# Optimization experiments

Hardware: AMD Instinct MI355X
Metric: run time of the kernel (lower is better)

Reference implementation:

```python
import jax, jax.numpy as jnp
import numpy as np

LN_EPS = 1e-5

def _layer_norm(x, g, b):
    mu = jnp.mean(x, axis=-1, keepdims=True)
    var = jnp.mean(jnp.square(x - mu), axis=-1, keepdims=True)
    return (x - mu) * jax.lax.rsqrt(var + LN_EPS) * g + b

def _conv(x, src, tgt, N, alphas, ws, W3, W_self, bias, deg_power):
    # alphas, ws: tuples of 3 per-edge [E] arrays (sp, ctx, lat)
    # W3: [3, in, out]; deg_power: [3]
    out = x @ W_self + bias  # self loop + bias, [N, out]
    for c in range(3):
        eff = alphas[c] * ws[c]                                   # [E]
        deg = jnp.ones((N,), x.dtype).at[tgt].add(eff)            # [N]
        dinv = jnp.power(jnp.clip(deg, 1e-6), deg_power[c])       # [N]
        norm = eff * dinv[tgt] * dinv[src]                        # [E]
        h = x @ W3[c]                                             # [N, out] (linear => transform before gather)
        msg = norm[:, None] * h[src]                              # [E, out]
        out = out + jax.ops.segment_sum(msg, tgt, num_segments=N)
    return out

def setup_inputs() -> dict:
    N, E, D, L = 50000, 1000000, 128, 2
    key = jax.random.key(0)
    ks = jax.random.split(key, 16)
    scale = 1.0 / np.sqrt(D)
    inp = {
        "x": jax.random.normal(ks[0], (N, D), jnp.float32),
        "edge_index": jax.random.randint(ks[1], (2, E), 0, N, jnp.int32),
        "alpha_sp": jax.random.uniform(ks[2], (E,), jnp.float32),
        "alpha_ctx": jax.random.uniform(ks[3], (E,), jnp.float32),
        "alpha_lat": jax.random.uniform(ks[4], (E,), jnp.float32),
        "w_sp": jax.random.uniform(ks[5], (E,), jnp.float32),
        "w_ctx": jax.random.uniform(ks[6], (E,), jnp.float32),
        "w_lat": jax.random.uniform(ks[7], (E,), jnp.float32),
        # stacked per-layer params: [L, 3, in, out] for the three channel weights
        "W3": jax.random.normal(ks[8], (L, 3, D, D), jnp.float32) * scale,
        "W_self": jax.random.normal(ks[9], (L, D, D), jnp.float32) * scale,
        "bias": jnp.zeros((L, D), jnp.float32),
        "deg_power": jnp.full((L, 3), -0.5, jnp.float32),
        "ln_g": jnp.ones((D,), jnp.float32),
        "ln_b": jnp.zeros((D,), jnp.float32),
        "num_nodes": N,
    }
    return inp

def reference(x, edge_index, alpha_sp, alpha_ctx, alpha_lat, w_sp, w_ctx, w_lat,
              W3, W_self, bias, deg_power, ln_g, ln_b, num_nodes):
    N = num_nodes
    src, tgt = edge_index[0], edge_index[1]
    alphas = (alpha_sp, alpha_ctx, alpha_lat)
    ws = (w_sp, w_ctx, w_lat)
    L = W3.shape[0]
    h = x
    for i in range(L):
        h = _conv(h, src, tgt, N, alphas, ws, W3[i], W_self[i], bias[i], deg_power[i])
        if i < L - 1:
            h = _layer_norm(h, ln_g, ln_b)
            h = jax.nn.relu(h)
            # dropout: eval mode (identity)
    return h
```

## Files before the change

kernel.cpp:

```cpp
#include <hip/hip_runtime.h>
#include <hip/hip_bf16.h>

typedef short bf16x8 __attribute__((ext_vector_type(8)));
typedef float f32x4 __attribute__((ext_vector_type(4)));

static inline int cdiv(int a, int b){ return (a + b - 1) / b; }

__device__ __forceinline__ unsigned pack_bf16_hi(float v){
    return ((unsigned)__bfloat16_as_ushort(__float2bfloat16(v))) << 16;
}
__device__ __forceinline__ float bf16hi_to_f32(unsigned bits_hi16){
    return __uint_as_float(bits_hi16);
}

__global__ void k_cnt(const int* __restrict__ tgt, int* __restrict__ cnt, int E){
    int e0 = (blockIdx.x * 256 + threadIdx.x) * 4;
    if (e0 + 3 < E){
        int4 t = *(const int4*)(tgt + e0);
        atomicAdd(&cnt[t.x], 1);
        atomicAdd(&cnt[t.y], 1);
        atomicAdd(&cnt[t.z], 1);
        atomicAdd(&cnt[t.w], 1);
    } else {
        for (int e = e0; e < E; ++e) atomicAdd(&cnt[tgt[e]], 1);
    }
}

__global__ void k_scan1(const int* __restrict__ cnt, int* __restrict__ rs,
                        int* __restrict__ bsum, int N){
    __shared__ int s[256];
    int i = blockIdx.x * 256 + threadIdx.x;
    int v = (i < N) ? cnt[i] : 0;
    s[threadIdx.x] = v;
    __syncthreads();
    for (int off = 1; off < 256; off <<= 1){
        int t = (threadIdx.x >= off) ? s[threadIdx.x - off] : 0;
        __syncthreads();
        s[threadIdx.x] += t;
        __syncthreads();
    }
    if (i < N) rs[i] = s[threadIdx.x] - v;
    if (threadIdx.x == 255) bsum[blockIdx.x] = s[255];
}

__global__ void k_scan2(int* __restrict__ bsum, int nb){
    __shared__ int s[256];
    int v = (threadIdx.x < nb) ? bsum[threadIdx.x] : 0;
    s[threadIdx.x] = v;
    __syncthreads();
    for (int off = 1; off < 256; off <<= 1){
        int t = (threadIdx.x >= off) ? s[threadIdx.x - off] : 0;
        __syncthreads();
        s[threadIdx.x] += t;
        __syncthreads();
    }
    if (threadIdx.x < nb) bsum[threadIdx.x] = s[threadIdx.x] - v;
}

__global__ void k_scan3(int* __restrict__ rs, int* __restrict__ nxt,
                        const int* __restrict__ bsum, int N, int E){
    int i = blockIdx.x * 256 + threadIdx.x;
    if (i < N){
        int v = rs[i] + bsum[blockIdx.x];
        rs[i] = v;
        nxt[i] = v;
    }
    if (i == 0) rs[N] = E;
}

__global__ void k_scatter(const int* __restrict__ src, const int* __restrict__ tgt,
                          const float* __restrict__ asp,
                          const float* __restrict__ actx,
                          const float* __restrict__ alat,
                          const float* __restrict__ wsp,
                          const float* __restrict__ wctx,
                          const float* __restrict__ wlat,
                          int* __restrict__ nxt,
                          uint2* __restrict__ effo, int E){
    int e = blockIdx.x * 256 + threadIdx.x;
    if (e >= E) return;
    int t = tgt[e];
    int pos = atomicAdd(&nxt[t], 1);
    uint2 v;
    v.x = (unsigned)src[e] | pack_bf16_hi(asp[e] * wsp[e]);
    v.y = (pack_bf16_hi(actx[e] * wctx[e]) >> 16) | pack_bf16_hi(alat[e] * wlat[e]);
    effo[pos] = v;
}

__global__ __launch_bounds__(256) void k_deg(
        const uint2* __restrict__ effo, const int* __restrict__ rs,
        const float* __restrict__ dp,
        float* __restrict__ dinv_all,
        int N, int L){
    int n = blockIdx.x * 256 + threadIdx.x;
    if (n >= N) return;
    int beg = rs[n], end = rs[n + 1];
    float s0 = 0.f, s1 = 0.f, s2 = 0.f;
    for (int i = beg; i < end; ++i){
        uint2 v = effo[i];
        s0 += bf16hi_to_f32(v.x & 0xFFFF0000u);
        s1 += bf16hi_to_f32(v.y << 16);
        s2 += bf16hi_to_f32(v.y & 0xFFFF0000u);
    }
    float d0 = fmaxf(1.f + s0, 1e-6f);
    float d1 = fmaxf(1.f + s1, 1e-6f);
    float d2 = fmaxf(1.f + s2, 1e-6f);
    for (int l = 0; l < L; ++l){
        size_t base = ((size_t)l * N + n) * 3;
        dinv_all[base + 0] = powf(d0, dp[l * 3 + 0]);
        dinv_all[base + 1] = powf(d1, dp[l * 3 + 1]);
        dinv_all[base + 2] = powf(d2, dp[l * 3 + 2]);
    }
}

__global__ void k_normv(const uint2* __restrict__ effo,
                        const float* __restrict__ dinv_all,
                        uint2* __restrict__ nv, int E, int N, int L){
    int i = blockIdx.x * 256 + threadIdx.x;
    if (i >= L * E) return;
    int l = i / E;
    int e = i - l * E;
    const float* dinv = dinv_all + (size_t)l * N * 3;
    uint2 v = effo[e];
    unsigned s = v.x & 0xFFFFu;
    float e0 = bf16hi_to_f32(v.x & 0xFFFF0000u);
    float e1 = bf16hi_to_f32(v.y << 16);
    float e2 = bf16hi_to_f32(v.y & 0xFFFF0000u);
    float n0 = e0 * dinv[3 * s + 0];
    float n1 = e1 * dinv[3 * s + 1];
    float n2 = e2 * dinv[3 * s + 2];
    uint2 o;
    o.x = s | pack_bf16_hi(n0);
    o.y = (pack_bf16_hi(n1) >> 16) | pack_bf16_hi(n2);
    nv[i] = o;
}

__global__ void k_x2bf(const float* __restrict__ x, __hip_bfloat16* __restrict__ Ap, int n){
    int i = blockIdx.x * 256 + threadIdx.x;
    if (i < n) Ap[(size_t)(i >> 7) * 512 + (i & 127)] = __float2bfloat16(x[i]);
}

__global__ void k_wcat(const float* __restrict__ Wself,
                       const float* __restrict__ W3,
                       __hip_bfloat16* __restrict__ BT,
                       int L){
    int i = blockIdx.x * 256 + threadIdx.x;
    if (i >= L * 65536) return;
    int l = i >> 16, r = i & 65535;
    int j = r >> 9, k = r & 511;
    float v;
    if (k < 128) v = Wself[l * 16384 + k * 128 + j];
    else {
        int c = (k >> 7) - 1, kk = k & 127;
        v = W3[l * 49152 + (c * 128 + kk) * 128 + j];
    }
    BT[i] = __float2bfloat16(v);
}

__global__ __launch_bounds__(256) void k_msg(
        __hip_bfloat16* __restrict__ Ap,
        const uint2* __restrict__ nv,
        const int* __restrict__ rs,
        const float* __restrict__ dinv,
        int N){
    int w = threadIdx.x >> 6, lane = threadIdx.x & 63;
    int t = blockIdx.x * 4 + w;
    if (t >= N) return;
    float ax0 = 0.f, ay0 = 0.f, ax1 = 0.f, ay1 = 0.f, ax2 = 0.f, ay2 = 0.f;
    int beg = rs[t], end = rs[t + 1];
    int i = beg;
    for (; i + 8 <= end; i += 8){
        uint2 m[8];
        #pragma unroll
        for (int u = 0; u < 8; ++u) m[u] = nv[i + u];
        float2 f[8];
        #pragma unroll
        for (int u = 0; u < 8; ++u){
            const __hip_bfloat162* p =
                (const __hip_bfloat162*)(Ap + (size_t)(m[u].x & 0xFFFFu) * 512);
            f[u] = __bfloat1622float2(p[lane]);
        }
        #pragma unroll
        for (int u = 0; u < 8; ++u){
            float n0 = bf16hi_to_f32(m[u].x & 0xFFFF0000u);
            float n1 = bf16hi_to_f32(m[u].y << 16);
            float n2 = bf16hi_to_f32(m[u].y & 0xFFFF0000u);
            ax0 += n0 * f[u].x; ay0 += n0 * f[u].y;
            ax1 += n1 * f[u].x; ay1 += n1 * f[u].y;
            ax2 += n2 * f[u].x; ay2 += n2 * f[u].y;
        }
    }
    for (; i < end; ++i){
        uint2 m = nv[i];
        const __hip_bfloat162* p =
            (const __hip_bfloat162*)(Ap + (size_t)(m.x & 0xFFFFu) * 512);
        float2 fv = __bfloat1622float2(p[lane]);
        float n0 = bf16hi_to_f32(m.x & 0xFFFF0000u);
        float n1 = bf16hi_to_f32(m.y << 16);
        float n2 = bf16hi_to_f32(m.y & 0xFFFF0000u);
        ax0 += n0 * fv.x; ay0 += n0 * fv.y;
        ax1 += n1 * fv.x; ay1 += n1 * fv.y;
        ax2 += n2 * fv.x; ay2 += n2 * fv.y;
    }
    float dt0 = dinv[3 * t], dt1 = dinv[3 * t + 1], dt2 = dinv[3 * t + 2];
    __hip_bfloat162* yo = (__hip_bfloat162*)(Ap + (size_t)t * 512 + 128) + lane;
    float2 r0 = {dt0 * ax0, dt0 * ay0};
    float2 r1 = {dt1 * ax1, dt1 * ay1};
    float2 r2 = {dt2 * ax2, dt2 * ay2};
    yo[0]   = __float22bfloat162_rn(r0);
    yo[64]  = __float22bfloat162_rn(r1);
    yo[128] = __float22bfloat162_rn(r2);
}

__global__ __launch_bounds__(256) void k_gemm(
        const __hip_bfloat16* __restrict__ A,
        const __hip_bfloat16* __restrict__ BT,
        const float* __restrict__ bias,
        float* __restrict__ outbuf,
        int M){
    __shared__ __hip_bfloat16 As[128 * 128];
    __shared__ __hip_bfloat16 Bs[128 * 128];
    const int tid = threadIdx.x;
    const int row0 = blockIdx.x * 128;
    const int w = tid >> 6, lane = tid & 63;
    const int wm = (w & 1) * 64, wn = (w >> 1) * 64;
    const int lm = lane & 15, lq = lane >> 4;

    f32x4 acc[4][4];
    #pragma unroll
    for (int mt = 0; mt < 4; ++mt)
        #pragma unroll
        for (int nt = 0; nt < 4; ++nt)
            acc[mt][nt] = {0.f, 0.f, 0.f, 0.f};

    for (int kt = 0; kt < 4; ++kt){
        #pragma unroll
        for (int it = 0; it < 8; ++it){
            int v = it * 256 + tid;
            int r = v >> 4, c = v & 15;
            int soff = r * 128 + ((c ^ (r & 15)) << 3);
            int4 av = {0, 0, 0, 0};
            if (row0 + r < M)
                av = *(const int4*)(A + (size_t)(row0 + r) * 512 + kt * 128 + (c << 3));
            *(int4*)(&As[soff]) = av;
            int4 bv = *(const int4*)(BT + (size_t)r * 512 + kt * 128 + (c << 3));
            *(int4*)(&Bs[soff]) = bv;
        }
        __syncthreads();

        #pragma unroll
        for (int kk = 0; kk < 4; ++kk){
            int kc = kk * 4 + lq;
            bf16x8 a[4], b[4];
            #pragma unroll
            for (int mt = 0; mt < 4; ++mt){
                int r = wm + mt * 16 + lm;
                a[mt] = *(const bf16x8*)(&As[r * 128 + ((kc ^ (r & 15)) << 3)]);
            }
            #pragma unroll
            for (int nt = 0; nt < 4; ++nt){
                int r = wn + nt * 16 + lm;
                b[nt] = *(const bf16x8*)(&Bs[r * 128 + ((kc ^ (r & 15)) << 3)]);
            }
            #pragma unroll
            for (int mt = 0; mt < 4; ++mt)
                #pragma unroll
                for (int nt = 0; nt < 4; ++nt)
                    acc[mt][nt] = __builtin_amdgcn_mfma_f32_16x16x32_bf16(
                        a[mt], b[nt], acc[mt][nt], 0, 0, 0);
        }
        __syncthreads();
    }

    #pragma unroll
    for (int mt = 0; mt < 4; ++mt){
        #pragma unroll
        for (int nt = 0; nt < 4; ++nt){
            int col = wn + nt * 16 + lm;
            #pragma unroll
            for (int r = 0; r < 4; ++r){
                int row = row0 + wm + mt * 16 + lq * 4 + r;
                if (row < M)
                    outbuf[(size_t)row * 128 + col] = acc[mt][nt][r] + bias[col];
            }
        }
    }
}

__global__ __launch_bounds__(256) void k_ln(
        const float* __restrict__ outbuf,
        const float* __restrict__ g,
        const float* __restrict__ b,
        __hip_bfloat16* __restrict__ Ap, int N){
    int w = threadIdx.x >> 6, lane = threadIdx.x & 63;
    int t = blockIdx.x * 4 + w;
    if (t >= N) return;
    const float* row = outbuf + (size_t)t * 128;
    float x0 = row[2 * lane], x1 = row[2 * lane + 1];
    float s = x0 + x1;
    #pragma unroll
    for (int off = 32; off; off >>= 1) s += __shfl_xor(s, off);
    float mu = s * (1.0f / 128.0f);
    float d0 = x0 - mu, d1 = x1 - mu;
    float ss = d0 * d0 + d1 * d1;
    #pragma unroll
    for (int off = 32; off; off >>= 1) ss += __shfl_xor(ss, off);
    float r = rsqrtf(ss * (1.0f / 128.0f) + 1e-5f);
    float y0 = fmaxf(d0 * r * g[2 * lane]     + b[2 * lane],     0.0f);
    float y1 = fmaxf(d1 * r * g[2 * lane + 1] + b[2 * lane + 1], 0.0f);
    float2 y = {y0, y1};
    *((__hip_bfloat162*)(Ap + (size_t)t * 512) + lane) = __float22bfloat162_rn(y);
}

extern "C" void kernel_launch(void* const* d_in, const int* in_sizes, int n_in,
                              void* d_out, int out_size, void* d_ws, size_t ws_size,
                              hipStream_t stream) {
    const float* x     = (const float*)d_in[0];
    const int*   ei    = (const int*)d_in[1];
    const float* asp   = (const float*)d_in[2];
    const float* actx  = (const float*)d_in[3];
    const float* alat  = (const float*)d_in[4];
    const float* wsp   = (const float*)d_in[5];
    const float* wctx  = (const float*)d_in[6];
    const float* wlat  = (const float*)d_in[7];
    const float* W3    = (const float*)d_in[8];
    const float* Wself = (const float*)d_in[9];
    const float* bias  = (const float*)d_in[10];
    const float* dpow  = (const float*)d_in[11];
    const float* lng   = (const float*)d_in[12];
    const float* lnb   = (const float*)d_in[13];

    const int N = in_sizes[0] / 128;
    const int E = in_sizes[1] / 2;
    const int L = in_sizes[8] / (3 * 128 * 128);
    const int* src = ei;
    const int* tgt = ei + E;

    char* p = (char*)d_ws;
    auto alloc = [&](size_t bytes) -> void* {
        void* r = (void*)p;
        p += (bytes + 255) & ~(size_t)255;
        return r;
    };
    int*   cnt      = (int*)  alloc((size_t)N * 4);
    int*   rs       = (int*)  alloc((size_t)(N + 1) * 4);
    int*   nxt      = (int*)  alloc((size_t)N * 4);
    int*   bsum     = (int*)  alloc(1024);
    uint2* effo     = (uint2*)alloc((size_t)E * 8);
    uint2* nv       = (uint2*)alloc((size_t)L * E * 8);
    float* dinv_all = (float*)alloc((size_t)L * N * 3 * 4);
    float* outbuf   = (float*)alloc((size_t)N * 128 * 4);
    __hip_bfloat16* Ap = (__hip_bfloat16*)alloc((size_t)N * 512 * 2);
    __hip_bfloat16* BT = (__hip_bfloat16*)alloc((size_t)L * 128 * 512 * 2);

    const int nb = cdiv(N, 256);

    hipMemsetAsync(cnt, 0, (size_t)N * 4, stream);
    k_cnt    <<<cdiv(E, 1024), 256, 0, stream>>>(tgt, cnt, E);
    k_scan1  <<<nb, 256, 0, stream>>>(cnt, rs, bsum, N);
    k_scan2  <<<1,  256, 0, stream>>>(bsum, nb);
    k_scan3  <<<nb, 256, 0, stream>>>(rs, nxt, bsum, N, E);
    k_scatter<<<cdiv(E, 256), 256, 0, stream>>>(src, tgt, asp, actx, alat, wsp, wctx, wlat,
                                                nxt, effo, E);
    k_deg    <<<cdiv(N, 256), 256, 0, stream>>>(effo, rs, dpow, dinv_all, N, L);
    k_x2bf   <<<cdiv(N * 128, 256), 256, 0, stream>>>(x, Ap, N * 128);
    k_wcat   <<<cdiv(L * 65536, 256), 256, 0, stream>>>(Wself, W3, BT, L);
    k_normv  <<<cdiv(L * E, 256), 256, 0, stream>>>(effo, dinv_all, nv, E, N, L);

    for (int l = 0; l < L; ++l){
        float* obuf = (l == L - 1) ? (float*)d_out : outbuf;
        const float* dinv_l = dinv_all + (size_t)l * N * 3;
        k_msg  <<<cdiv(N, 4), 256, 0, stream>>>(Ap, nv + (size_t)l * E, rs, dinv_l, N);
        k_gemm <<<cdiv(N, 128), 256, 0, stream>>>(Ap, BT + (size_t)l * 65536,
                                                  bias + l * 128, obuf, N);
        if (l < L - 1)
            k_ln<<<cdiv(N, 4), 256, 0, stream>>>(obuf, lng, lnb, Ap, N);
    }
}
```

Before: 416.8 us.

## Build CSR with two-level bucketed counting sort instead of global atomics

Replaces per-node global atomic counting, the three-pass scan and the atomic scatter with a two-level binning sort. Edges are first binned into 128-node buckets using shared-memory histograms and staged, locally coalesced writes, then each bucket is sorted by target in shared memory and the row starts are written out. The aim is to remove the scattered global atomics and uncoalesced writes of CSR construction. The cost is extra passes and an intermediate 16-byte-per-edge buffer that reuses the nv workspace, and the code hardcodes a limit of 1024 buckets.

```diff
diff --git a/kernel.cpp b/kernel.cpp
--- a/kernel.cpp
+++ b/kernel.cpp
@@ -4,6 +4,9 @@
 typedef short bf16x8 __attribute__((ext_vector_type(8)));
 typedef float f32x4 __attribute__((ext_vector_type(4)));
 
+#define BSH 7
+#define BK  (1 << BSH)
+
 static inline int cdiv(int a, int b){ return (a + b - 1) / b; }
 
 __device__ __forceinline__ unsigned pack_bf16_hi(float v){
@@ -13,78 +16,150 @@
     return __uint_as_float(bits_hi16);
 }
 
-__global__ void k_cnt(const int* __restrict__ tgt, int* __restrict__ cnt, int E){
-    int e0 = (blockIdx.x * 256 + threadIdx.x) * 4;
-    if (e0 + 3 < E){
-        int4 t = *(const int4*)(tgt + e0);
-        atomicAdd(&cnt[t.x], 1);
-        atomicAdd(&cnt[t.y], 1);
-        atomicAdd(&cnt[t.z], 1);
-        atomicAdd(&cnt[t.w], 1);
-    } else {
-        for (int e = e0; e < E; ++e) atomicAdd(&cnt[tgt[e]], 1);
-    }
-}
-
-__global__ void k_scan1(const int* __restrict__ cnt, int* __restrict__ rs,
-                        int* __restrict__ bsum, int N){
-    __shared__ int s[256];
-    int i = blockIdx.x * 256 + threadIdx.x;
-    int v = (i < N) ? cnt[i] : 0;
-    s[threadIdx.x] = v;
+__global__ __launch_bounds__(256) void k_bcnt0(const int* __restrict__ tgt,
+                                               int* __restrict__ gcnt, int E, int NB){
+    __shared__ int lh[1024];
+    int tid = threadIdx.x;
+    for (int b = tid; b < 1024; b += 256) lh[b] = 0;
+    __syncthreads();
+    int c0 = blockIdx.x * 4096;
+    #pragma unroll
+    for (int u = 0; u < 16; ++u){
+        int e = c0 + u * 256 + tid;
+        if (e < E) atomicAdd(&lh[tgt[e] >> BSH], 1);
+    }
+    __syncthreads();
+    for (int b = tid; b < NB; b += 256){
+        int c = lh[b];
+        if (c) atomicAdd(&gcnt[b], c);
+    }
+}
+
+__global__ __launch_bounds__(256) void k_bscan(const int* __restrict__ gcnt,
+                                               int* __restrict__ bbase,
+                                               int* __restrict__ gcur,
+                                               int* __restrict__ rs,
+                                               int N, int E){
+    __shared__ int sc[256];
+    int tid = threadIdx.x;
+    int b0 = tid * 4;
+    int v0 = gcnt[b0], v1 = gcnt[b0 + 1], v2 = gcnt[b0 + 2], v3 = gcnt[b0 + 3];
+    int t3 = v0 + v1 + v2 + v3;
+    sc[tid] = t3;
     __syncthreads();
     for (int off = 1; off < 256; off <<= 1){
-        int t = (threadIdx.x >= off) ? s[threadIdx.x - off] : 0;
-        __syncthreads();
-        s[threadIdx.x] += t;
-        __syncthreads();
-    }
-    if (i < N) rs[i] = s[threadIdx.x] - v;
-    if (threadIdx.x == 255) bsum[blockIdx.x] = s[255];
-}
-
-__global__ void k_scan2(int* __restrict__ bsum, int nb){
-    __shared__ int s[256];
-    int v = (threadIdx.x < nb) ? bsum[threadIdx.x] : 0;
-    s[threadIdx.x] = v;
+        int x = (tid >= off) ? sc[tid - off] : 0;
+        __syncthreads();
+        sc[tid] += x;
+        __syncthreads();
+    }
+    int ex = sc[tid] - t3;
+    bbase[b0]     = ex;
+    bbase[b0 + 1] = ex + v0;
+    bbase[b0 + 2] = ex + v0 + v1;
+    bbase[b0 + 3] = ex + v0 + v1 + v2;
+    gcur[b0] = bbase[b0]; gcur[b0 + 1] = bbase[b0 + 1];
+    gcur[b0 + 2] = bbase[b0 + 2]; gcur[b0 + 3] = bbase[b0 + 3];
+    if (tid == 255) bbase[1024] = sc[255];
+    if (tid == 0)   rs[N] = E;
+}
+
+__global__ __launch_bounds__(256) void k_bin(
+        const int* __restrict__ src, const int* __restrict__ tgt,
+        const float* __restrict__ asp, const float* __restrict__ actx,
+        const float* __restrict__ alat, const float* __restrict__ wsp,
+        const float* __restrict__ wctx, const float* __restrict__ wlat,
+        int* __restrict__ gcur, uint4* __restrict__ binned, int E, int NB){
+    __shared__ int lh[1024], lo[1024], lc[1024], gb[1024], tsum[256];
+    __shared__ unsigned sx[4096], sy[4096];
+    __shared__ int st[4096];
+    int tid = threadIdx.x;
+    int c0 = blockIdx.x * 4096;
+    int cnt = E - c0; if (cnt > 4096) cnt = 4096;
+    for (int b = tid; b < 1024; b += 256){ lh[b] = 0; lc[b] = 0; }
+    __syncthreads();
+    #pragma unroll
+    for (int u = 0; u < 16; ++u){
+        int e = c0 + u * 256 + tid;
+        if (e < E) atomicAdd(&lh[tgt[e] >> BSH], 1);
+    }
+    __syncthreads();
+    int b4 = tid * 4;
+    int v0 = lh[b4], v1 = lh[b4 + 1], v2 = lh[b4 + 2], v3 = lh[b4 + 3];
+    int t3 = v0 + v1 + v2 + v3;
+    tsum[tid] = t3;
     __syncthreads();
     for (int off = 1; off < 256; off <<= 1){
-        int t = (threadIdx.x >= off) ? s[threadIdx.x - off] : 0;
-        __syncthreads();
-        s[threadIdx.x] += t;
-        __syncthreads();
-    }
-    if (threadIdx.x < nb) bsum[threadIdx.x] = s[threadIdx.x] - v;
-}
-
-__global__ void k_scan3(int* __restrict__ rs, int* __restrict__ nxt,
-                        const int* __restrict__ bsum, int N, int E){
-    int i = blockIdx.x * 256 + threadIdx.x;
-    if (i < N){
-        int v = rs[i] + bsum[blockIdx.x];
-        rs[i] = v;
-        nxt[i] = v;
-    }
-    if (i == 0) rs[N] = E;
-}
-
-__global__ void k_scatter(const int* __restrict__ src, const int* __restrict__ tgt,
-                          const float* __restrict__ asp,
-                          const float* __restrict__ actx,
-                          const float* __restrict__ alat,
-                          const float* __restrict__ wsp,
-                          const float* __restrict__ wctx,
-                          const float* __restrict__ wlat,
-                          int* __restrict__ nxt,
-                          uint2* __restrict__ effo, int E){
-    int e = blockIdx.x * 256 + threadIdx.x;
-    if (e >= E) return;
-    int t = tgt[e];
-    int pos = atomicAdd(&nxt[t], 1);
-    uint2 v;
-    v.x = (unsigned)src[e] | pack_bf16_hi(asp[e] * wsp[e]);
-    v.y = (pack_bf16_hi(actx[e] * wctx[e]) >> 16) | pack_bf16_hi(alat[e] * wlat[e]);
-    effo[pos] = v;
+        int x = (tid >= off) ? tsum[tid - off] : 0;
+        __syncthreads();
+        tsum[tid] += x;
+        __syncthreads();
+    }
+    int ex = tsum[tid] - t3;
+    lo[b4] = ex; lo[b4 + 1] = ex + v0; lo[b4 + 2] = ex + v0 + v1; lo[b4 + 3] = ex + v0 + v1 + v2;
+    for (int b = tid; b < NB; b += 256){
+        int c = lh[b];
+        gb[b] = c ? atomicAdd(&gcur[b], c) : 0;
+    }
+    __syncthreads();
+    #pragma unroll
+    for (int u = 0; u < 16; ++u){
+        int e = c0 + u * 256 + tid;
+        if (e < E){
+            int t = tgt[e];
+            int b = t >> BSH;
+            int p = lo[b] + atomicAdd(&lc[b], 1);
+            sx[p] = (unsigned)src[e] | pack_bf16_hi(asp[e] * wsp[e]);
+            sy[p] = (pack_bf16_hi(actx[e] * wctx[e]) >> 16) | pack_bf16_hi(alat[e] * wlat[e]);
+            st[p] = t;
+        }
+    }
+    __syncthreads();
+    for (int i = tid; i < cnt; i += 256){
+        int t = st[i];
+        int b = t >> BSH;
+        int g = gb[b] + (i - lo[b]);
+        uint4 o = {sx[i], sy[i], (unsigned)t, 0u};
+        binned[g] = o;
+    }
+}
+
+__global__ __launch_bounds__(256) void k_bucket(
+        const uint4* __restrict__ binned, const int* __restrict__ bbase,
+        uint2* __restrict__ effo, int* __restrict__ rs, int N){
+    __shared__ int th[128], sc2[128], cur[128];
+    int tid = threadIdx.x;
+    int b = blockIdx.x;
+    int t0 = b << BSH;
+    int ebeg = bbase[b], eend = bbase[b + 1];
+    if (tid < 128) th[tid] = 0;
+    __syncthreads();
+    for (int i = ebeg + tid; i < eend; i += 256)
+        atomicAdd(&th[(int)binned[i].z - t0], 1);
+    __syncthreads();
+    int v = (tid < 128) ? th[tid] : 0;
+    if (tid < 128) sc2[tid] = v;
+    __syncthreads();
+    for (int off = 1; off < 128; off <<= 1){
+        int x = (tid >= off && tid < 128) ? sc2[tid - off] : 0;
+        __syncthreads();
+        if (tid < 128) sc2[tid] += x;
+        __syncthreads();
+    }
+    if (tid < 128){
+        int exv = sc2[tid] - v;
+        cur[tid] = exv;
+        int t = t0 + tid;
+        if (t < N) rs[t] = ebeg + exv;
+    }
+    __syncthreads();
+    for (int i = ebeg + tid; i < eend; i += 256){
+        uint4 r = binned[i];
+        int loc = (int)r.z - t0;
+        int p = atomicAdd(&cur[loc], 1);
+        uint2 o = {r.x, r.y};
+        effo[ebeg + p] = o;
+    }
 }
 
 __global__ __launch_bounds__(256) void k_deg(
@@ -333,6 +408,7 @@
     const int N = in_sizes[0] / 128;
     const int E = in_sizes[1] / 2;
     const int L = in_sizes[8] / (3 * 128 * 128);
+    const int NB = cdiv(N, BK);
     const int* src = ei;
     const int* tgt = ei + E;
 
@@ -342,37 +418,35 @@
         p += (bytes + 255) & ~(size_t)255;
         return r;
     };
-    int*   cnt      = (int*)  alloc((size_t)N * 4);
     int*   rs       = (int*)  alloc((size_t)(N + 1) * 4);
-    int*   nxt      = (int*)  alloc((size_t)N * 4);
-    int*   bsum     = (int*)  alloc(1024);
+    int*   gcnt     = (int*)  alloc(1024 * 4);
+    int*   bbase    = (int*)  alloc(1025 * 4);
+    int*   gcur     = (int*)  alloc(1024 * 4);
     uint2* effo     = (uint2*)alloc((size_t)E * 8);
     uint2* nv       = (uint2*)alloc((size_t)L * E * 8);
     float* dinv_all = (float*)alloc((size_t)L * N * 3 * 4);
     float* outbuf   = (float*)alloc((size_t)N * 128 * 4);
     __hip_bfloat16* Ap = (__hip_bfloat16*)alloc((size_t)N * 512 * 2);
     __hip_bfloat16* BT = (__hip_bfloat16*)alloc((size_t)L * 128 * 512 * 2);
-
-    const int nb = cdiv(N, 256);
-
-    hipMemsetAsync(cnt, 0, (size_t)N * 4, stream);
-    k_cnt    <<<cdiv(E, 1024), 256, 0, stream>>>(tgt, cnt, E);
-    k_scan1  <<<nb, 256, 0, stream>>>(cnt, rs, bsum, N);
-    k_scan2  <<<1,  256, 0, stream>>>(bsum, nb);
-    k_scan3  <<<nb, 256, 0, stream>>>(rs, nxt, bsum, N, E);
-    k_scatter<<<cdiv(E, 256), 256, 0, stream>>>(src, tgt, asp, actx, alat, wsp, wctx, wlat,
-                                                nxt, effo, E);
-    k_deg    <<<cdiv(N, 256), 256, 0, stream>>>(effo, rs, dpow, dinv_all, N, L);
-    k_x2bf   <<<cdiv(N * 128, 256), 256, 0, stream>>>(x, Ap, N * 128);
-    k_wcat   <<<cdiv(L * 65536, 256), 256, 0, stream>>>(Wself, W3, BT, L);
-    k_normv  <<<cdiv(L * E, 256), 256, 0, stream>>>(effo, dinv_all, nv, E, N, L);
+    uint4* binned = (uint4*)nv;
+
+    hipMemsetAsync(gcnt, 0, 1024 * 4, stream);
+    k_bcnt0 <<<cdiv(E, 4096), 256, 0, stream>>>(tgt, gcnt, E, NB);
+    k_bscan <<<1, 256, 0, stream>>>(gcnt, bbase, gcur, rs, N, E);
+    k_bin   <<<cdiv(E, 4096), 256, 0, stream>>>(src, tgt, asp, actx, alat, wsp, wctx, wlat,
+                                                gcur, binned, E, NB);
+    k_bucket<<<NB, 256, 0, stream>>>(binned, bbase, effo, rs, N);
+    k_deg   <<<cdiv(N, 256), 256, 0, stream>>>(effo, rs, dpow, dinv_all, N, L);
+    k_x2bf  <<<cdiv(N * 128, 256), 256, 0, stream>>>(x, Ap, N * 128);
+    k_wcat  <<<cdiv(L * 65536, 256), 256, 0, stream>>>(Wself, W3, BT, L);
+    k_normv <<<cdiv(L * E, 256), 256, 0, stream>>>(effo, dinv_all, nv, E, N, L);
 
     for (int l = 0; l < L; ++l){
         float* obuf = (l == L - 1) ? (float*)d_out : outbuf;
         const float* dinv_l = dinv_all + (size_t)l * N * 3;
-        k_msg  <<<cdiv(N, 4), 256, 0, stream>>>(Ap, nv + (size_t)l * E, rs, dinv_l, N);
-        k_gemm <<<cdiv(N, 128), 256, 0, stream>>>(Ap, BT + (size_t)l * 65536,
-                                                  bias + l * 128, obuf, N);
+        k_msg <<<cdiv(N, 4), 256, 0, stream>>>(Ap, nv + (size_t)l * E, rs, dinv_l, N);
+        k_gemm<<<cdiv(N, 128), 256, 0, stream>>>(Ap, BT + (size_t)l * 65536,
+                                                 bias + l * 128, obuf, N);
         if (l < L - 1)
             k_ln<<<cdiv(N, 4), 256, 0, stream>>>(obuf, lng, lnb, Ap, N);
     }
```

New measurement: 371.1 us. -10.9%, faster.
